# Kernel tuning notes

Measured on AMD Instinct MI355X. Metric: run time of the kernel, lower is better.

Reference implementation:

```python
import jax, jax.numpy as jnp
import numpy as np

NUM_POINTS = 1_000_000
WINDOW = 8                      # 2^3 corner stencil for linear shape functions in 3D
GRID = (128, 128, 128)
NUM_CELLS = GRID[0] * GRID[1] * GRID[2]
CELL = 1.0 / 64.0
INV_CELL = 64.0
ORIGIN = jnp.zeros((3,), dtype=jnp.float32)
# forward_window: the 8 corner offsets of the enclosing cell
FWD_WINDOW = jnp.array([[i, j, k] for i in (0, 1) for j in (0, 1) for k in (0, 1)],
                       dtype=jnp.int32)  # [8,3]


def setup_inputs() -> dict:
    key = jax.random.key(0)
    k1, k2, k3 = jax.random.split(key, 3)
    domain = GRID[0] * CELL
    # keep particles one cell away from the boundary so all stencil hashes are in range
    pos = jax.random.uniform(k1, (NUM_POINTS, 3), dtype=jnp.float32) * (domain - 2 * CELL) + CELL
    vel = jax.random.normal(k2, (NUM_POINTS, 3), dtype=jnp.float32)
    mass = jax.random.uniform(k3, (NUM_POINTS,), dtype=jnp.float32) * 1e-3 + 1e-4
    return {"position_stack": pos, "velocity_stack": vel, "mass_stack": mass}


def reference(position_stack, velocity_stack, mass_stack):
    # ---- get_interactions: gather particle pos, hash into grid, shape functions ----
    rel = (position_stack - ORIGIN) * INV_CELL               # [N,3] position in cell units
    base = jnp.floor(rel)                                    # [N,3]
    grid_pos = base[:, None, :] + FWD_WINDOW[None, :, :].astype(rel.dtype)  # [N,8,3]
    dist = rel[:, None, :] - grid_pos                        # [N,8,3], each dim in (-1,1)

    gp = grid_pos.astype(jnp.int32)
    # get_hash, dim==3: pos[2] + pos[0]*grid[2] + pos[1]*grid[2]*grid[0]
    intr_hash = gp[..., 2] + gp[..., 0] * GRID[2] + gp[..., 1] * (GRID[2] * GRID[0])  # [N,8]

    # linear shape function: N = prod_d (1 - |x_d|); grad scaled by inv_cell_size
    w = 1.0 - jnp.abs(dist)                                  # [N,8,3]
    shapef = w[..., 0] * w[..., 1] * w[..., 2]               # [N,8]
    valid = (intr_hash >= 0) & (intr_hash < NUM_CELLS)
    shapef = jnp.where(valid, shapef, 0.0)

    g0 = -jnp.sign(dist[..., 0]) * w[..., 1] * w[..., 2]
    g1 = -jnp.sign(dist[..., 1]) * w[..., 0] * w[..., 2]
    g2 = -jnp.sign(dist[..., 2]) * w[..., 0] * w[..., 1]
    shapef_grad = jnp.stack([g0, g1, g2], axis=-1) * INV_CELL  # [N,8,3]
    shapef_grad = jnp.where(valid[..., None], shapef_grad, 0.0)

    # intr_dist_padded = -dist * cell_size (kept implicitly via dist; used in APIC-style p2g)
    # ---- p2g scatter (vmap_intr_scatter semantics): mass & momentum to grid nodes ----
    h_flat = jnp.clip(intr_hash, 0, NUM_CELLS - 1).reshape(-1)  # [N*8]
    sm = shapef * mass_stack[:, None]                           # [N,8]
    node_mass = jax.ops.segment_sum(sm.reshape(-1), h_flat, num_segments=NUM_CELLS)   # [C]
    mom = sm[..., None] * velocity_stack[:, None, :]            # [N,8,3]
    node_mom = jax.ops.segment_sum(mom.reshape(-1, 3), h_flat, num_segments=NUM_CELLS)  # [C,3]

    return jnp.concatenate([node_mass[:, None], node_mom], axis=1)  # [C,4]
```

## Files before the change

kernel.cpp:

```cpp
#include <hip/hip_runtime.h>
#include <hip/hip_fp16.h>


#define GRID_DIM   128
#define NUM_CELLS  (GRID_DIM * GRID_DIM * GRID_DIM)
#define INV_CELL   64.0f
#define OVF_MAX    65536
#define SCAN_BLKS  2048

#define TDIM4      32
#define NTILES4    (TDIM4 * TDIM4 * TDIM4)
#define NXCD       8
#define XCAP       16
#define MAXCAP     3
#define NSEG       216
#define NREC       2369
#define EPAD(sc)   ((sc) * 3 + ((sc) >> 2))

typedef float floatx4 __attribute__((ext_vector_type(4)));

__device__ __forceinline__ int cell_id(int ix, int iy, int iz) {
    return iz + ix * GRID_DIM + iy * (GRID_DIM * GRID_DIM);
}

__device__ __forceinline__ unsigned int q16(float f) {
    int q = (int)(f * 65536.0f + 0.5f);
    return (unsigned int)min(q, 65535);
}
__device__ __forceinline__ unsigned int f2h(float f) {
    return (unsigned int)__half_as_ushort(__float2half(f));
}
__device__ __forceinline__ float h2f(unsigned int b) {
    return __half2float(__ushort_as_half((unsigned short)(b & 0xffffu)));
}

__global__ __launch_bounds__(256) void xcd_place_kernel(
    const float* __restrict__ pos, const float* __restrict__ vel,
    const float* __restrict__ mass, unsigned int* __restrict__ tile_cnt,
    uint4* __restrict__ lists, int* __restrict__ ovf_cnt,
    int* __restrict__ ovf_list, int n)
{
    int xcd = blockIdx.x & (NXCD - 1);
    int i0 = blockIdx.x * 512 + threadIdx.x;
    #pragma unroll
    for (int k = 0; k < 2; ++k) {
        int i = i0 + k * 256;
        if (i < n) {
            float px = __builtin_nontemporal_load(&pos[3 * i + 0]);
            float py = __builtin_nontemporal_load(&pos[3 * i + 1]);
            float pz = __builtin_nontemporal_load(&pos[3 * i + 2]);
            float rx = px * INV_CELL, ry = py * INV_CELL, rz = pz * INV_CELL;
            float bx = floorf(rx), by = floorf(ry), bz = floorf(rz);
            float fx = rx - bx, fy = ry - by, fz = rz - bz;
            int ix = min(max((int)bx, 0), GRID_DIM - 1);
            int iy = min(max((int)by, 0), GRID_DIM - 1);
            int iz = min(max((int)bz, 0), GRID_DIM - 1);
            int tile = (iz >> 2) | ((ix >> 2) << 5) | ((iy >> 2) << 10);
            int sub = (xcd << 15) | tile;
            unsigned int s = atomicAdd(&tile_cnt[sub], 1u);
            if (s < (unsigned int)XCAP) {
                float m  = __builtin_nontemporal_load(&mass[i]);
                float vx = __builtin_nontemporal_load(&vel[3 * i + 0]);
                float vy = __builtin_nontemporal_load(&vel[3 * i + 1]);
                float vz = __builtin_nontemporal_load(&vel[3 * i + 2]);
                unsigned int lid = (unsigned int)((iz & 3) | ((ix & 3) << 2)
                                                           | ((iy & 3) << 4));
                uint4 r;
                r.x = q16(fx) | (q16(fy) << 16);
                r.y = q16(fz) | (f2h(m) << 16);
                r.z = f2h(vx) | (f2h(vy) << 16);
                r.w = f2h(vz) | (lid << 16);
                lists[(size_t)sub * XCAP + (int)s] = r;
            } else {
                int o = atomicAdd(ovf_cnt, 1);
                if (o < OVF_MAX) ovf_list[o] = i;
            }
        }
    }
}

__global__ __launch_bounds__(512) void xcd_gather_kernel(
    const uint4* __restrict__ lists, const unsigned int* __restrict__ tile_cnt,
    float4* __restrict__ out)
{
    __shared__ float4 recA[NREC];
    __shared__ unsigned int recB[NREC];
    __shared__ unsigned int cnt_s[729];
    __shared__ unsigned short seg_off[218];
    __shared__ int wtot[8];
    __shared__ int ovf_n;
    __shared__ short ovf_sc[64];
    __shared__ uint4 ovf_rec[64];

    int tid = threadIdx.x;
    int swz = (blockIdx.x & 7) * 512 + (blockIdx.x >> 3);
    int bz = swz & 15;
    int bx = (swz >> 4) & 15;
    int by = swz >> 8;
    int g0x = bx * 8, g0y = by * 8, g0z = bz * 8;
    int Tz0 = bz * 2 - 1, Tx0 = bx * 2 - 1, Ty0 = by * 2 - 1;

    for (int s2 = tid; s2 < 729; s2 += 512) cnt_s[s2] = 0;
    if (tid == 0) ovf_n = 0;

    unsigned int c = 0;
    if (tid < NSEG) {
        int xcd = tid & 7, q = tid >> 3;
        int ltz = q % 3, q2 = q / 3, ltx = q2 % 3, lty = q2 / 3;
        int tz_ = Tz0 + ltz, tx_ = Tx0 + ltx, ty_ = Ty0 + lty;
        if ((tz_ >= 0) & (tx_ >= 0) & (ty_ >= 0)) {
            int tile = tz_ | (tx_ << 5) | (ty_ << 10);
            c = min(tile_cnt[(xcd << 15) | tile], (unsigned int)XCAP);
        }
    }
    unsigned int v = c;
    #pragma unroll
    for (int d = 1; d < 64; d <<= 1) {
        unsigned int t = __shfl_up(v, d, 64);
        if ((tid & 63) >= d) v += t;
    }
    if ((tid & 63) == 63) wtot[tid >> 6] = (int)v;
    __syncthreads();
    if (tid == 0) {
        int run = 0;
        #pragma unroll
        for (int w2 = 0; w2 < 8; ++w2) { int t = wtot[w2]; wtot[w2] = run; run += t; }
    }
    __syncthreads();
    if (tid <= NSEG)
        seg_off[tid] = (unsigned short)((unsigned int)wtot[tid >> 6] + v - c);
    __syncthreads();
    int R = (int)seg_off[NSEG];

    for (int r = tid; r < R; r += 512) {
        int s = 0;
        #pragma unroll
        for (int step = 128; step >= 1; step >>= 1)
            if (s + step <= NSEG && (int)seg_off[s + step] <= r) s += step;
        int xcd = s & 7, q = s >> 3;
        int ltz = q % 3, q2 = q / 3, ltx = q2 % 3, lty = q2 / 3;
        int tz_ = Tz0 + ltz, tx_ = Tx0 + ltx, ty_ = Ty0 + lty;
        int tile = tz_ | (tx_ << 5) | (ty_ << 10);
        int j = r - (int)seg_off[s];
        uint4 rec = lists[(size_t)((xcd << 15) | tile) * XCAP + j];
        unsigned int lid = rec.w >> 16;
        int cz = tz_ * 4 + (int)(lid & 3u);
        int cx = tx_ * 4 + (int)((lid >> 2) & 3u);
        int cy = ty_ * 4 + (int)(lid >> 4);
        int uz = cz - (g0z - 1), ux = cx - (g0x - 1), uy = cy - (g0y - 1);
        if (((unsigned)uz < 9u) & ((unsigned)ux < 9u) & ((unsigned)uy < 9u)) {
            int sc = uy * 81 + ux * 9 + uz;
            unsigned int j2 = atomicAdd(&cnt_s[sc], 1u);
            if (j2 < MAXCAP) {
                int e = EPAD(sc) + (int)j2;
                float fx = (float)(rec.x & 0xffffu) * (1.0f / 65536.0f);
                float fy = (float)(rec.x >> 16)     * (1.0f / 65536.0f);
                float fz = (float)(rec.y & 0xffffu) * (1.0f / 65536.0f);
                recA[e] = make_float4(fx, fy, fz, __uint_as_float(rec.z));
                recB[e] = (rec.y >> 16) | (rec.w << 16);
            } else {
                int o = atomicAdd(&ovf_n, 1);
                if (o < 64) { ovf_sc[o] = (short)sc; ovf_rec[o] = rec; }
            }
        }
    }
    __syncthreads();

    int tz = tid & 7, tx = (tid >> 3) & 7, ty = tid >> 6;
    float a0 = 0.0f, a1 = 0.0f, a2 = 0.0f, a3 = 0.0f;

    #pragma unroll
    for (int dy = 0; dy < 2; ++dy) {
        #pragma unroll
        for (int dx = 0; dx < 2; ++dx) {
            int scb = (ty + dy) * 81 + (tx + dx) * 9 + tz;
            #pragma unroll
            for (int dz = 0; dz < 2; ++dz) {
                int sc = scb + dz;
                int cnt = min((int)cnt_s[sc], MAXCAP);
                int eb = EPAD(sc);
                for (int j = 0; j < cnt; ++j) {
                    float4 A = recA[eb + j];
                    unsigned int B = recB[eb + j];
                    unsigned int w3 = __float_as_uint(A.w);
                    float wx = dx ? (1.0f - A.x) : A.x;
                    float wy = dy ? (1.0f - A.y) : A.y;
                    float wz = dz ? (1.0f - A.z) : A.z;
                    float sm = wx * wy * wz * h2f(B);
                    a0 += sm;
                    a1 += sm * h2f(w3);
                    a2 += sm * h2f(w3 >> 16);
                    a3 += sm * h2f(B >> 16);
                }
            }
        }
    }

    int no = min(ovf_n, 64);
    for (int e2 = 0; e2 < no; ++e2) {
        int sc = (int)ovf_sc[e2];
        int uzv = sc % 9, t2 = sc / 9, uxv = t2 % 9, uyv = t2 / 9;
        int ddz = uzv - tz, ddx = uxv - tx, ddy = uyv - ty;
        if (((unsigned)ddz < 2u) & ((unsigned)ddx < 2u) & ((unsigned)ddy < 2u)) {
            uint4 rec = ovf_rec[e2];
            float fx = (float)(rec.x & 0xffffu) * (1.0f / 65536.0f);
            float fy = (float)(rec.x >> 16)     * (1.0f / 65536.0f);
            float fz = (float)(rec.y & 0xffffu) * (1.0f / 65536.0f);
            float wx = ddx ? (1.0f - fx) : fx;
            float wy = ddy ? (1.0f - fy) : fy;
            float wz = ddz ? (1.0f - fz) : fz;
            float sm = wx * wy * wz * h2f(rec.y >> 16);
            a0 += sm;
            a1 += sm * h2f(rec.z);
            a2 += sm * h2f(rec.z >> 16);
            a3 += sm * h2f(rec.w);
        }
    }

    int id = (g0z + tz) + (g0x + tx) * GRID_DIM
           + (g0y + ty) * (GRID_DIM * GRID_DIM);
    floatx4 vv = { a0, a1, a2, a3 };
    __builtin_nontemporal_store(vv, (floatx4*)&out[id]);
}

__global__ __launch_bounds__(256) void fixup_kernel(
    const float* __restrict__ pos, const float* __restrict__ vel,
    const float* __restrict__ mass, const int* __restrict__ ovf_cnt,
    const int* __restrict__ ovf_list, float* __restrict__ out)
{
    int total = min(*ovf_cnt, OVF_MAX);
    for (int k = blockIdx.x * 256 + threadIdx.x; k < total; k += gridDim.x * 256) {
        int i = ovf_list[k];
        float px = pos[3 * i + 0] * INV_CELL;
        float py = pos[3 * i + 1] * INV_CELL;
        float pz = pos[3 * i + 2] * INV_CELL;
        float bx = floorf(px), by = floorf(py), bz = floorf(pz);
        float fx = px - bx, fy = py - by, fz = pz - bz;
        int ix = (int)bx, iy = (int)by, iz = (int)bz;
        float m = mass[i];
        float vx = vel[3 * i + 0], vy = vel[3 * i + 1], vz = vel[3 * i + 2];
        float wx[2] = { 1.0f - fx, fx }, wy[2] = { 1.0f - fy, fy }, wz[2] = { 1.0f - fz, fz };
        #pragma unroll
        for (int a = 0; a < 2; ++a)
            #pragma unroll
            for (int b = 0; b < 2; ++b)
                #pragma unroll
                for (int c = 0; c < 2; ++c) {
                    int h = cell_id(ix + a, iy + b, iz + c);
                    bool valid = (h >= 0) && (h < NUM_CELLS);
                    int hc = min(max(h, 0), NUM_CELLS - 1);
                    float s = valid ? (wx[a] * wy[b] * wz[c]) : 0.0f;
                    float sm = s * m;
                    float* cell = out + 4 * (size_t)hc;
                    atomicAdd(cell + 0, sm);
                    atomicAdd(cell + 1, sm * vx);
                    atomicAdd(cell + 2, sm * vy);
                    atomicAdd(cell + 3, sm * vz);
                }
    }
}

__global__ __launch_bounds__(256) void s_hist_kernel(
    const float* __restrict__ pos, int* __restrict__ counts, int n)
{
    int i = blockIdx.x * 256 + threadIdx.x;
    if (i >= n) return;
    int ix = min(max((int)floorf(pos[3 * i + 0] * INV_CELL), 0), GRID_DIM - 1);
    int iy = min(max((int)floorf(pos[3 * i + 1] * INV_CELL), 0), GRID_DIM - 1);
    int iz = min(max((int)floorf(pos[3 * i + 2] * INV_CELL), 0), GRID_DIM - 1);
    atomicAdd(&counts[cell_id(ix, iy, iz)], 1);
}

__global__ __launch_bounds__(256) void s_scan_partials_kernel(
    const int* __restrict__ counts, int* __restrict__ partials)
{
    __shared__ int red[256];
    int t = threadIdx.x;
    int4 v = ((const int4*)counts)[blockIdx.x * 256 + t];
    red[t] = v.x + v.y + v.z + v.w;
    __syncthreads();
    for (int off = 128; off > 0; off >>= 1) {
        if (t < off) red[t] += red[t + off];
        __syncthreads();
    }
    if (t == 0) partials[blockIdx.x] = red[0];
}

__global__ __launch_bounds__(1024) void s_scan_tops_kernel(int* __restrict__ partials)
{
    __shared__ int s[1024];
    int t = threadIdx.x;
    int p0 = partials[2 * t], p1 = partials[2 * t + 1];
    int sum = p0 + p1;
    s[t] = sum;
    __syncthreads();
    for (int off = 1; off < 1024; off <<= 1) {
        int x = (t >= off) ? s[t - off] : 0;
        __syncthreads();
        s[t] += x;
        __syncthreads();
    }
    int excl = s[t] - sum;
    partials[2 * t] = excl;
    partials[2 * t + 1] = excl + p0;
}

__global__ __launch_bounds__(256) void s_scan_final_kernel(
    const int* __restrict__ counts, const int* __restrict__ partials,
    int* __restrict__ offsets, int* __restrict__ cursors)
{
    __shared__ int s[256];
    int t = threadIdx.x;
    int g = blockIdx.x * 256 + t;
    int4 v = ((const int4*)counts)[g];
    int sum = v.x + v.y + v.z + v.w;
    s[t] = sum;
    __syncthreads();
    for (int off = 1; off < 256; off <<= 1) {
        int x = (t >= off) ? s[t - off] : 0;
        __syncthreads();
        s[t] += x;
        __syncthreads();
    }
    int run = partials[blockIdx.x] + s[t] - sum;
    int4 o = make_int4(run, run + v.x, run + v.x + v.y, run + v.x + v.y + v.z);
    ((int4*)offsets)[g] = o;
    ((int4*)cursors)[g] = o;
}

__global__ __launch_bounds__(256) void s_binplace_kernel(
    const float* __restrict__ pos, const float* __restrict__ vel,
    const float* __restrict__ mass, int* __restrict__ cursors,
    float4* __restrict__ records, int n)
{
    int i = blockIdx.x * 256 + threadIdx.x;
    if (i >= n) return;
    float rx = pos[3 * i + 0] * INV_CELL;
    float ry = pos[3 * i + 1] * INV_CELL;
    float rz = pos[3 * i + 2] * INV_CELL;
    int ix = min(max((int)floorf(rx), 0), GRID_DIM - 1);
    int iy = min(max((int)floorf(ry), 0), GRID_DIM - 1);
    int iz = min(max((int)floorf(rz), 0), GRID_DIM - 1);
    int slot = atomicAdd(&cursors[cell_id(ix, iy, iz)], 1);
    records[2 * slot + 0] = make_float4(rx, ry, rz, mass[i]);
    records[2 * slot + 1] = make_float4(vel[3 * i + 0], vel[3 * i + 1],
                                        vel[3 * i + 2], 0.0f);
}

__global__ __launch_bounds__(256) void s_node_gather_kernel(
    const float4* __restrict__ records, const int* __restrict__ offsets,
    const int* __restrict__ cursors, float4* __restrict__ out)
{
    int id = blockIdx.x * 256 + threadIdx.x;
    int gz = id & (GRID_DIM - 1);
    int gx = (id >> 7) & (GRID_DIM - 1);
    int gy = id >> 14;
    float fgx = (float)gx, fgy = (float)gy, fgz = (float)gz;
    float a0 = 0.0f, a1 = 0.0f, a2 = 0.0f, a3 = 0.0f;
    int z0 = max(gz - 1, 0), y0 = max(gy - 1, 0), x0 = max(gx - 1, 0);
    for (int cy = y0; cy <= gy; ++cy) {
        for (int cx = x0; cx <= gx; ++cx) {
            int cb = cx * GRID_DIM + cy * (GRID_DIM * GRID_DIM);
            int beg = offsets[cb + z0];
            int end = cursors[cb + gz];
            for (int p = beg; p < end; ++p) {
                float4 r0 = records[2 * p + 0];
                float4 r1 = records[2 * p + 1];
                float w = (1.0f - fabsf(r0.x - fgx)) *
                          (1.0f - fabsf(r0.y - fgy)) *
                          (1.0f - fabsf(r0.z - fgz));
                float sm = w * r0.w;
                a0 += sm; a1 += sm * r1.x; a2 += sm * r1.y; a3 += sm * r1.z;
            }
        }
    }
    out[id] = make_float4(a0, a1, a2, a3);
}

__global__ __launch_bounds__(256) void p2g_scatter_kernel(
    const float* __restrict__ pos, const float* __restrict__ vel,
    const float* __restrict__ mass, float* __restrict__ out, int n)
{
    int i = blockIdx.x * blockDim.x + threadIdx.x;
    if (i >= n) return;
    float px = pos[3 * i + 0] * INV_CELL;
    float py = pos[3 * i + 1] * INV_CELL;
    float pz = pos[3 * i + 2] * INV_CELL;
    float bx = floorf(px), by = floorf(py), bz = floorf(pz);
    float fx = px - bx, fy = py - by, fz = pz - bz;
    int ix = (int)bx, iy = (int)by, iz = (int)bz;
    float m = mass[i];
    float vx = vel[3 * i + 0], vy = vel[3 * i + 1], vz = vel[3 * i + 2];
    float wx[2] = { 1.0f - fx, fx }, wy[2] = { 1.0f - fy, fy }, wz[2] = { 1.0f - fz, fz };
    #pragma unroll
    for (int a = 0; a < 2; ++a)
        #pragma unroll
        for (int b = 0; b < 2; ++b)
            #pragma unroll
            for (int c = 0; c < 2; ++c) {
                int h = cell_id(ix + a, iy + b, iz + c);
                bool valid = (h >= 0) && (h < NUM_CELLS);
                int hc = min(max(h, 0), NUM_CELLS - 1);
                float s = valid ? (wx[a] * wy[b] * wz[c]) : 0.0f;
                float sm = s * m;
                float* cell = out + 4 * (size_t)hc;
                atomicAdd(cell + 0, sm);
                atomicAdd(cell + 1, sm * vx);
                atomicAdd(cell + 2, sm * vy);
                atomicAdd(cell + 3, sm * vz);
            }
}

extern "C" void kernel_launch(void* const* d_in, const int* in_sizes, int n_in,
                              void* d_out, int out_size, void* d_ws, size_t ws_size,
                              hipStream_t stream) {
    const float* pos  = (const float*)d_in[0];
    const float* vel  = (const float*)d_in[1];
    const float* mass = (const float*)d_in[2];
    float* out = (float*)d_out;
    int n = in_sizes[2];
    int blocks = (n + 255) / 256;

    size_t x_off_lists = (size_t)NXCD * NTILES4 * 4;
    size_t x_off_ovf   = x_off_lists + (size_t)NXCD * NTILES4 * XCAP * 16;
    size_t need_xcd    = x_off_ovf + 256 + (size_t)OVF_MAX * 4;

    size_t s_off_offsets  = (size_t)NUM_CELLS * 4;
    size_t s_off_records  = s_off_offsets + (size_t)NUM_CELLS * 4;
    size_t s_off_partials = s_off_records + (size_t)n * 32;
    size_t need_sorted    = s_off_partials + (size_t)SCAN_BLKS * 4;

    if (ws_size >= need_xcd) {
        char* ws = (char*)d_ws;
        unsigned int* tile_cnt = (unsigned int*)ws;
        uint4* lists  = (uint4*)(ws + x_off_lists);
        int* ovf_cnt  = (int*)(ws + x_off_ovf);
        int* ovf_list = ovf_cnt + 64;

        (void)hipMemsetAsync(tile_cnt, 0, x_off_lists, stream);
        (void)hipMemsetAsync(ovf_cnt, 0, 4, stream);
        xcd_place_kernel<<<(n + 511) / 512, 256, 0, stream>>>(
            pos, vel, mass, tile_cnt, lists, ovf_cnt, ovf_list, n);
        xcd_gather_kernel<<<NTILES4 / 8, 512, 0, stream>>>(
            lists, tile_cnt, (float4*)out);
        fixup_kernel<<<32, 256, 0, stream>>>(pos, vel, mass, ovf_cnt,
                                             ovf_list, out);
    } else if (ws_size >= need_sorted) {
        char* ws = (char*)d_ws;
        int* counts   = (int*)ws;
        int* offsets  = (int*)(ws + s_off_offsets);
        float4* records = (float4*)(ws + s_off_records);
        int* partials = (int*)(ws + s_off_partials);

        (void)hipMemsetAsync(counts, 0, (size_t)NUM_CELLS * 4, stream);
        s_hist_kernel<<<blocks, 256, 0, stream>>>(pos, counts, n);
        s_scan_partials_kernel<<<SCAN_BLKS, 256, 0, stream>>>(counts, partials);
        s_scan_tops_kernel<<<1, 1024, 0, stream>>>(partials);
        s_scan_final_kernel<<<SCAN_BLKS, 256, 0, stream>>>(counts, partials,
                                                           offsets, counts);
        s_binplace_kernel<<<blocks, 256, 0, stream>>>(pos, vel, mass, counts,
                                                      records, n);
        s_node_gather_kernel<<<NUM_CELLS / 256, 256, 0, stream>>>(
            records, offsets, counts, (float4*)out);
    } else {
        (void)hipMemsetAsync(out, 0, (size_t)out_size * sizeof(float), stream);
        p2g_scatter_kernel<<<blocks, 256, 0, stream>>>(pos, vel, mass, out, n);
    }
}
```

Before: 175.7 us.

## Replace fixed-capacity tile lists with counting-sort dense lists via histogram and scan

Replaces the per-(XCD,tile) fixed 16-slot lists, and the overflow list with its atomic fixup kernel, with a counting sort. A histogram pass over positions is followed by a three-kernel prefix scan and a placement pass into densely packed records. The gather kernel reads each segment's base offset and count from the offsets and cursors arrays. This removes the overflow path and shrinks the list footprint from a padded 16-slot-per-tile array to one record per particle. In exchange it adds a second pass over the positions and four more kernel launches.

After: 206.7 us. +17.6%, slower.

```diff
diff --git a/kernel.cpp b/kernel.cpp
--- a/kernel.cpp
+++ b/kernel.cpp
@@ -5,13 +5,12 @@
 #define GRID_DIM   128
 #define NUM_CELLS  (GRID_DIM * GRID_DIM * GRID_DIM)
 #define INV_CELL   64.0f
-#define OVF_MAX    65536
 #define SCAN_BLKS  2048
 
 #define TDIM4      32
 #define NTILES4    (TDIM4 * TDIM4 * TDIM4)
 #define NXCD       8
-#define XCAP       16
+#define NSUB       (NXCD * NTILES4)
 #define MAXCAP     3
 #define NSEG       216
 #define NREC       2369
@@ -34,59 +33,119 @@
     return __half2float(__ushort_as_half((unsigned short)(b & 0xffffu)));
 }
 
-__global__ __launch_bounds__(256) void xcd_place_kernel(
+__global__ __launch_bounds__(256) void x_hist_kernel(
+    const float* __restrict__ pos, unsigned int* __restrict__ tile_cnt, int n)
+{
+    int xcd = blockIdx.x & (NXCD - 1);
+    int i = blockIdx.x * 256 + threadIdx.x;
+    if (i >= n) return;
+    float px = __builtin_nontemporal_load(&pos[3 * i + 0]);
+    float py = __builtin_nontemporal_load(&pos[3 * i + 1]);
+    float pz = __builtin_nontemporal_load(&pos[3 * i + 2]);
+    int ix = min(max((int)floorf(px * INV_CELL), 0), GRID_DIM - 1);
+    int iy = min(max((int)floorf(py * INV_CELL), 0), GRID_DIM - 1);
+    int iz = min(max((int)floorf(pz * INV_CELL), 0), GRID_DIM - 1);
+    int tile = (iz >> 2) | ((ix >> 2) << 5) | ((iy >> 2) << 10);
+    atomicAdd(&tile_cnt[(xcd << 15) | tile], 1u);
+}
+
+__global__ __launch_bounds__(256) void x_scan_partials(
+    const unsigned int* __restrict__ cnt, unsigned int* __restrict__ partials)
+{
+    __shared__ unsigned int red[256];
+    int t = threadIdx.x;
+    uint4 v = ((const uint4*)cnt)[blockIdx.x * 256 + t];
+    red[t] = v.x + v.y + v.z + v.w;
+    __syncthreads();
+    for (int off = 128; off > 0; off >>= 1) {
+        if (t < off) red[t] += red[t + off];
+        __syncthreads();
+    }
+    if (t == 0) partials[blockIdx.x] = red[0];
+}
+
+__global__ __launch_bounds__(256) void x_scan_tops(unsigned int* __restrict__ partials)
+{
+    __shared__ unsigned int s[256];
+    int t = threadIdx.x;
+    unsigned int p = partials[t];
+    s[t] = p;
+    __syncthreads();
+    for (int off = 1; off < 256; off <<= 1) {
+        unsigned int x = (t >= off) ? s[t - off] : 0;
+        __syncthreads();
+        s[t] += x;
+        __syncthreads();
+    }
+    partials[t] = s[t] - p;
+}
+
+__global__ __launch_bounds__(256) void x_scan_final(
+    const unsigned int* __restrict__ cnt, const unsigned int* __restrict__ partials,
+    unsigned int* __restrict__ offsets, unsigned int* __restrict__ cursors)
+{
+    __shared__ unsigned int s[256];
+    int t = threadIdx.x;
+    int g = blockIdx.x * 256 + t;
+    uint4 v = ((const uint4*)cnt)[g];
+    unsigned int sum = v.x + v.y + v.z + v.w;
+    s[t] = sum;
+    __syncthreads();
+    for (int off = 1; off < 256; off <<= 1) {
+        unsigned int x = (t >= off) ? s[t - off] : 0;
+        __syncthreads();
+        s[t] += x;
+        __syncthreads();
+    }
+    unsigned int run = partials[blockIdx.x] + s[t] - sum;
+    uint4 o = make_uint4(run, run + v.x, run + v.x + v.y, run + v.x + v.y + v.z);
+    ((uint4*)offsets)[g] = o;
+    ((uint4*)cursors)[g] = o;
+}
+
+__global__ __launch_bounds__(256) void xcd_binplace_kernel(
     const float* __restrict__ pos, const float* __restrict__ vel,
-    const float* __restrict__ mass, unsigned int* __restrict__ tile_cnt,
-    uint4* __restrict__ lists, int* __restrict__ ovf_cnt,
-    int* __restrict__ ovf_list, int n)
+    const float* __restrict__ mass, unsigned int* __restrict__ cursors,
+    uint4* __restrict__ lists, int n)
 {
     int xcd = blockIdx.x & (NXCD - 1);
-    int i0 = blockIdx.x * 512 + threadIdx.x;
-    #pragma unroll
-    for (int k = 0; k < 2; ++k) {
-        int i = i0 + k * 256;
-        if (i < n) {
-            float px = __builtin_nontemporal_load(&pos[3 * i + 0]);
-            float py = __builtin_nontemporal_load(&pos[3 * i + 1]);
-            float pz = __builtin_nontemporal_load(&pos[3 * i + 2]);
-            float rx = px * INV_CELL, ry = py * INV_CELL, rz = pz * INV_CELL;
-            float bx = floorf(rx), by = floorf(ry), bz = floorf(rz);
-            float fx = rx - bx, fy = ry - by, fz = rz - bz;
-            int ix = min(max((int)bx, 0), GRID_DIM - 1);
-            int iy = min(max((int)by, 0), GRID_DIM - 1);
-            int iz = min(max((int)bz, 0), GRID_DIM - 1);
-            int tile = (iz >> 2) | ((ix >> 2) << 5) | ((iy >> 2) << 10);
-            int sub = (xcd << 15) | tile;
-            unsigned int s = atomicAdd(&tile_cnt[sub], 1u);
-            if (s < (unsigned int)XCAP) {
-                float m  = __builtin_nontemporal_load(&mass[i]);
-                float vx = __builtin_nontemporal_load(&vel[3 * i + 0]);
-                float vy = __builtin_nontemporal_load(&vel[3 * i + 1]);
-                float vz = __builtin_nontemporal_load(&vel[3 * i + 2]);
-                unsigned int lid = (unsigned int)((iz & 3) | ((ix & 3) << 2)
-                                                           | ((iy & 3) << 4));
-                uint4 r;
-                r.x = q16(fx) | (q16(fy) << 16);
-                r.y = q16(fz) | (f2h(m) << 16);
-                r.z = f2h(vx) | (f2h(vy) << 16);
-                r.w = f2h(vz) | (lid << 16);
-                lists[(size_t)sub * XCAP + (int)s] = r;
-            } else {
-                int o = atomicAdd(ovf_cnt, 1);
-                if (o < OVF_MAX) ovf_list[o] = i;
-            }
-        }
-    }
+    int i = blockIdx.x * 256 + threadIdx.x;
+    if (i >= n) return;
+    float px = __builtin_nontemporal_load(&pos[3 * i + 0]);
+    float py = __builtin_nontemporal_load(&pos[3 * i + 1]);
+    float pz = __builtin_nontemporal_load(&pos[3 * i + 2]);
+    float rx = px * INV_CELL, ry = py * INV_CELL, rz = pz * INV_CELL;
+    float bx = floorf(rx), by = floorf(ry), bz = floorf(rz);
+    float fx = rx - bx, fy = ry - by, fz = rz - bz;
+    int ix = min(max((int)bx, 0), GRID_DIM - 1);
+    int iy = min(max((int)by, 0), GRID_DIM - 1);
+    int iz = min(max((int)bz, 0), GRID_DIM - 1);
+    int tile = (iz >> 2) | ((ix >> 2) << 5) | ((iy >> 2) << 10);
+    int sub = (xcd << 15) | tile;
+    unsigned int s = atomicAdd(&cursors[sub], 1u);
+    float m  = __builtin_nontemporal_load(&mass[i]);
+    float vx = __builtin_nontemporal_load(&vel[3 * i + 0]);
+    float vy = __builtin_nontemporal_load(&vel[3 * i + 1]);
+    float vz = __builtin_nontemporal_load(&vel[3 * i + 2]);
+    unsigned int lid = (unsigned int)((iz & 3) | ((ix & 3) << 2)
+                                               | ((iy & 3) << 4));
+    uint4 r;
+    r.x = q16(fx) | (q16(fy) << 16);
+    r.y = q16(fz) | (f2h(m) << 16);
+    r.z = f2h(vx) | (f2h(vy) << 16);
+    r.w = f2h(vz) | (lid << 16);
+    lists[s] = r;
 }
 
 __global__ __launch_bounds__(512) void xcd_gather_kernel(
-    const uint4* __restrict__ lists, const unsigned int* __restrict__ tile_cnt,
-    float4* __restrict__ out)
+    const uint4* __restrict__ lists, const unsigned int* __restrict__ offsets,
+    const unsigned int* __restrict__ cursors, float4* __restrict__ out)
 {
     __shared__ float4 recA[NREC];
     __shared__ unsigned int recB[NREC];
     __shared__ unsigned int cnt_s[729];
-    __shared__ unsigned short seg_off[218];
+    __shared__ unsigned int seg_base[NSEG];
+    __shared__ unsigned int seg_off[218];
     __shared__ int wtot[8];
     __shared__ int ovf_n;
     __shared__ short ovf_sc[64];
@@ -103,14 +162,15 @@
     for (int s2 = tid; s2 < 729; s2 += 512) cnt_s[s2] = 0;
     if (tid == 0) ovf_n = 0;
 
-    unsigned int c = 0;
+    unsigned int c = 0, base = 0;
     if (tid < NSEG) {
         int xcd = tid & 7, q = tid >> 3;
         int ltz = q % 3, q2 = q / 3, ltx = q2 % 3, lty = q2 / 3;
         int tz_ = Tz0 + ltz, tx_ = Tx0 + ltx, ty_ = Ty0 + lty;
         if ((tz_ >= 0) & (tx_ >= 0) & (ty_ >= 0)) {
-            int tile = tz_ | (tx_ << 5) | (ty_ << 10);
-            c = min(tile_cnt[(xcd << 15) | tile], (unsigned int)XCAP);
+            int sub = (xcd << 15) | (tz_ | (tx_ << 5) | (ty_ << 10));
+            base = offsets[sub];
+            c = cursors[sub] - base;
         }
     }
     unsigned int v = c;
@@ -128,7 +188,8 @@
     }
     __syncthreads();
     if (tid <= NSEG)
-        seg_off[tid] = (unsigned short)((unsigned int)wtot[tid >> 6] + v - c);
+        seg_off[tid] = (unsigned int)wtot[tid >> 6] + v - c;
+    if (tid < NSEG) seg_base[tid] = base;
     __syncthreads();
     int R = (int)seg_off[NSEG];
 
@@ -137,12 +198,11 @@
         #pragma unroll
         for (int step = 128; step >= 1; step >>= 1)
             if (s + step <= NSEG && (int)seg_off[s + step] <= r) s += step;
-        int xcd = s & 7, q = s >> 3;
+        int q = s >> 3;
         int ltz = q % 3, q2 = q / 3, ltx = q2 % 3, lty = q2 / 3;
         int tz_ = Tz0 + ltz, tx_ = Tx0 + ltx, ty_ = Ty0 + lty;
-        int tile = tz_ | (tx_ << 5) | (ty_ << 10);
         int j = r - (int)seg_off[s];
-        uint4 rec = lists[(size_t)((xcd << 15) | tile) * XCAP + j];
+        uint4 rec = lists[seg_base[s] + j];
         unsigned int lid = rec.w >> 16;
         int cz = tz_ * 4 + (int)(lid & 3u);
         int cx = tx_ * 4 + (int)((lid >> 2) & 3u);
@@ -221,43 +281,6 @@
            + (g0y + ty) * (GRID_DIM * GRID_DIM);
     floatx4 vv = { a0, a1, a2, a3 };
     __builtin_nontemporal_store(vv, (floatx4*)&out[id]);
-}
-
-__global__ __launch_bounds__(256) void fixup_kernel(
-    const float* __restrict__ pos, const float* __restrict__ vel,
-    const float* __restrict__ mass, const int* __restrict__ ovf_cnt,
-    const int* __restrict__ ovf_list, float* __restrict__ out)
-{
-    int total = min(*ovf_cnt, OVF_MAX);
-    for (int k = blockIdx.x * 256 + threadIdx.x; k < total; k += gridDim.x * 256) {
-        int i = ovf_list[k];
-        float px = pos[3 * i + 0] * INV_CELL;
-        float py = pos[3 * i + 1] * INV_CELL;
-        float pz = pos[3 * i + 2] * INV_CELL;
-        float bx = floorf(px), by = floorf(py), bz = floorf(pz);
-        float fx = px - bx, fy = py - by, fz = pz - bz;
-        int ix = (int)bx, iy = (int)by, iz = (int)bz;
-        float m = mass[i];
-        float vx = vel[3 * i + 0], vy = vel[3 * i + 1], vz = vel[3 * i + 2];
-        float wx[2] = { 1.0f - fx, fx }, wy[2] = { 1.0f - fy, fy }, wz[2] = { 1.0f - fz, fz };
-        #pragma unroll
-        for (int a = 0; a < 2; ++a)
-            #pragma unroll
-            for (int b = 0; b < 2; ++b)
-                #pragma unroll
-                for (int c = 0; c < 2; ++c) {
-                    int h = cell_id(ix + a, iy + b, iz + c);
-                    bool valid = (h >= 0) && (h < NUM_CELLS);
-                    int hc = min(max(h, 0), NUM_CELLS - 1);
-                    float s = valid ? (wx[a] * wy[b] * wz[c]) : 0.0f;
-                    float sm = s * m;
-                    float* cell = out + 4 * (size_t)hc;
-                    atomicAdd(cell + 0, sm);
-                    atomicAdd(cell + 1, sm * vx);
-                    atomicAdd(cell + 2, sm * vy);
-                    atomicAdd(cell + 3, sm * vz);
-                }
-    }
 }
 
 __global__ __launch_bounds__(256) void s_hist_kernel(
@@ -421,30 +444,35 @@
     int n = in_sizes[2];
     int blocks = (n + 255) / 256;
 
-    size_t x_off_lists = (size_t)NXCD * NTILES4 * 4;
-    size_t x_off_ovf   = x_off_lists + (size_t)NXCD * NTILES4 * XCAP * 16;
-    size_t need_xcd    = x_off_ovf + 256 + (size_t)OVF_MAX * 4;
+    size_t x_off_offsets  = (size_t)NSUB * 4;
+    size_t x_off_cursors  = x_off_offsets + (size_t)NSUB * 4;
+    size_t x_off_partials = x_off_cursors + (size_t)NSUB * 4;
+    size_t x_off_lists    = x_off_partials + 4096;
+    size_t need_dense     = x_off_lists + (size_t)n * 16;
 
     size_t s_off_offsets  = (size_t)NUM_CELLS * 4;
     size_t s_off_records  = s_off_offsets + (size_t)NUM_CELLS * 4;
     size_t s_off_partials = s_off_records + (size_t)n * 32;
     size_t need_sorted    = s_off_partials + (size_t)SCAN_BLKS * 4;
 
-    if (ws_size >= need_xcd) {
+    if (ws_size >= need_dense) {
         char* ws = (char*)d_ws;
         unsigned int* tile_cnt = (unsigned int*)ws;
-        uint4* lists  = (uint4*)(ws + x_off_lists);
-        int* ovf_cnt  = (int*)(ws + x_off_ovf);
-        int* ovf_list = ovf_cnt + 64;
-
-        (void)hipMemsetAsync(tile_cnt, 0, x_off_lists, stream);
-        (void)hipMemsetAsync(ovf_cnt, 0, 4, stream);
-        xcd_place_kernel<<<(n + 511) / 512, 256, 0, stream>>>(
-            pos, vel, mass, tile_cnt, lists, ovf_cnt, ovf_list, n);
+        unsigned int* offsets  = (unsigned int*)(ws + x_off_offsets);
+        unsigned int* cursors  = (unsigned int*)(ws + x_off_cursors);
+        unsigned int* partials = (unsigned int*)(ws + x_off_partials);
+        uint4* lists           = (uint4*)(ws + x_off_lists);
+
+        (void)hipMemsetAsync(tile_cnt, 0, (size_t)NSUB * 4, stream);
+        x_hist_kernel<<<blocks, 256, 0, stream>>>(pos, tile_cnt, n);
+        x_scan_partials<<<NSUB / 1024, 256, 0, stream>>>(tile_cnt, partials);
+        x_scan_tops<<<1, 256, 0, stream>>>(partials);
+        x_scan_final<<<NSUB / 1024, 256, 0, stream>>>(tile_cnt, partials,
+                                                      offsets, cursors);
+        xcd_binplace_kernel<<<blocks, 256, 0, stream>>>(
+            pos, vel, mass, cursors, lists, n);
         xcd_gather_kernel<<<NTILES4 / 8, 512, 0, stream>>>(
-            lists, tile_cnt, (float4*)out);
-        fixup_kernel<<<32, 256, 0, stream>>>(pos, vel, mass, ovf_cnt,
-                                             ovf_list, out);
+            lists, offsets, cursors, (float4*)out);
     } else if (ws_size >= need_sorted) {
         char* ws = (char*)d_ws;
         int* counts   = (int*)ws;
```

## Replace per-XCD tile lists with two-pass region binning and in-region tile sort

Applied to the files above, without the earlier changes.

Drops the per-XCD 4^3 tile lists, which used scattered global atomics and fixed-capacity slots. Each block now bins 4096 particles into 512 coarse 16^3-cell regions in LDS and writes them to global region buffers in contiguous chunks, with one global atomic per region per block. A second kernel sorts each region's records into 64 tiles, so the gather reads 27 contiguous segments instead of 216 small per-XCD lists. Overflow records are stored packed, so fixup no longer re-reads the original inputs. The cost is an extra kernel pass that reads and writes all records, plus heavy LDS use.

After: 163.5 us. -6.9%, faster.

```diff
diff --git a/kernel.cpp b/kernel.cpp
--- a/kernel.cpp
+++ b/kernel.cpp
@@ -8,12 +8,11 @@
 #define OVF_MAX    65536
 #define SCAN_BLKS  2048
 
-#define TDIM4      32
-#define NTILES4    (TDIM4 * TDIM4 * TDIM4)
-#define NXCD       8
-#define XCAP       16
+#define NREG       512
+#define RCAP       2560
+#define PPB        4096
 #define MAXCAP     3
-#define NSEG       216
+#define NSEG       27
 #define NREC       2369
 #define EPAD(sc)   ((sc) * 3 + ((sc) >> 2))
 
@@ -34,18 +33,34 @@
     return __half2float(__ushort_as_half((unsigned short)(b & 0xffffu)));
 }
 
-__global__ __launch_bounds__(256) void xcd_place_kernel(
+__global__ __launch_bounds__(1024) void region_bin_kernel(
     const float* __restrict__ pos, const float* __restrict__ vel,
-    const float* __restrict__ mass, unsigned int* __restrict__ tile_cnt,
-    uint4* __restrict__ lists, int* __restrict__ ovf_cnt,
-    int* __restrict__ ovf_list, int n)
-{
-    int xcd = blockIdx.x & (NXCD - 1);
-    int i0 = blockIdx.x * 512 + threadIdx.x;
+    const float* __restrict__ mass, unsigned int* __restrict__ region_cursor,
+    uint4* __restrict__ regbuf, int* __restrict__ ovf_cnt,
+    uint4* __restrict__ ovf_rec, unsigned int* __restrict__ ovf_reg, int n)
+{
+    __shared__ uint4 rec_lds[PPB];
+    __shared__ unsigned short regof[PPB];
+    __shared__ unsigned int cnt[NREG];
+    __shared__ unsigned int lofs[NREG];
+    __shared__ unsigned int gbase[NREG];
+    __shared__ unsigned int wtot[8];
+
+    int tid = threadIdx.x;
+    int base_i = blockIdx.x * PPB;
+    int blockn = min(PPB, n - base_i);
+
+    if (tid < NREG) cnt[tid] = 0;
+    __syncthreads();
+
+    uint4 r_[4]; int reg_[4], rank_[4], val_[4];
     #pragma unroll
-    for (int k = 0; k < 2; ++k) {
-        int i = i0 + k * 256;
-        if (i < n) {
+    for (int k = 0; k < 4; ++k) {
+        int e = k * 1024 + tid;
+        int i = base_i + e;
+        val_[k] = (e < blockn);
+        reg_[k] = 0; rank_[k] = 0;
+        if (val_[k]) {
             float px = __builtin_nontemporal_load(&pos[3 * i + 0]);
             float py = __builtin_nontemporal_load(&pos[3 * i + 1]);
             float pz = __builtin_nontemporal_load(&pos[3 * i + 2]);
@@ -55,39 +70,137 @@
             int ix = min(max((int)bx, 0), GRID_DIM - 1);
             int iy = min(max((int)by, 0), GRID_DIM - 1);
             int iz = min(max((int)bz, 0), GRID_DIM - 1);
-            int tile = (iz >> 2) | ((ix >> 2) << 5) | ((iy >> 2) << 10);
-            int sub = (xcd << 15) | tile;
-            unsigned int s = atomicAdd(&tile_cnt[sub], 1u);
-            if (s < (unsigned int)XCAP) {
-                float m  = __builtin_nontemporal_load(&mass[i]);
-                float vx = __builtin_nontemporal_load(&vel[3 * i + 0]);
-                float vy = __builtin_nontemporal_load(&vel[3 * i + 1]);
-                float vz = __builtin_nontemporal_load(&vel[3 * i + 2]);
-                unsigned int lid = (unsigned int)((iz & 3) | ((ix & 3) << 2)
-                                                           | ((iy & 3) << 4));
-                uint4 r;
-                r.x = q16(fx) | (q16(fy) << 16);
-                r.y = q16(fz) | (f2h(m) << 16);
-                r.z = f2h(vx) | (f2h(vy) << 16);
-                r.w = f2h(vz) | (lid << 16);
-                lists[(size_t)sub * XCAP + (int)s] = r;
-            } else {
-                int o = atomicAdd(ovf_cnt, 1);
-                if (o < OVF_MAX) ovf_list[o] = i;
-            }
-        }
-    }
-}
-
-__global__ __launch_bounds__(512) void xcd_gather_kernel(
-    const uint4* __restrict__ lists, const unsigned int* __restrict__ tile_cnt,
+            int reg = (iz >> 4) | ((ix >> 4) << 3) | ((iy >> 4) << 6);
+            unsigned int cid = (unsigned int)((iz & 15) | ((ix & 15) << 4)
+                                                        | ((iy & 15) << 8));
+            float m  = __builtin_nontemporal_load(&mass[i]);
+            float vx = __builtin_nontemporal_load(&vel[3 * i + 0]);
+            float vy = __builtin_nontemporal_load(&vel[3 * i + 1]);
+            float vz = __builtin_nontemporal_load(&vel[3 * i + 2]);
+            uint4 r;
+            r.x = q16(fx) | (q16(fy) << 16);
+            r.y = q16(fz) | (f2h(m) << 16);
+            r.z = f2h(vx) | (f2h(vy) << 16);
+            r.w = f2h(vz) | (cid << 16);
+            r_[k] = r;
+            reg_[k] = reg;
+            rank_[k] = (int)atomicAdd(&cnt[reg], 1u);
+        }
+    }
+    __syncthreads();
+
+    unsigned int c = 0, v = 0;
+    if (tid < NREG) {
+        c = cnt[tid];
+        v = c;
+        #pragma unroll
+        for (int d = 1; d < 64; d <<= 1) {
+            unsigned int t = __shfl_up(v, d, 64);
+            if ((tid & 63) >= d) v += t;
+        }
+        if ((tid & 63) == 63) wtot[tid >> 6] = v;
+    }
+    __syncthreads();
+    if (tid == 0) {
+        unsigned int run = 0;
+        #pragma unroll
+        for (int w = 0; w < 8; ++w) { unsigned int t = wtot[w]; wtot[w] = run; run += t; }
+    }
+    __syncthreads();
+    if (tid < NREG) {
+        lofs[tid] = wtot[tid >> 6] + v - c;
+        if (c) gbase[tid] = atomicAdd(&region_cursor[tid], c);
+    }
+    __syncthreads();
+
+    #pragma unroll
+    for (int k = 0; k < 4; ++k) {
+        if (val_[k]) {
+            int d = (int)lofs[reg_[k]] + rank_[k];
+            rec_lds[d] = r_[k];
+            regof[d] = (unsigned short)reg_[k];
+        }
+    }
+    __syncthreads();
+
+    for (int e = tid; e < blockn; e += 1024) {
+        uint4 rr = rec_lds[e];
+        int rg = (int)regof[e];
+        unsigned int slot = gbase[rg] + (unsigned int)(e - (int)lofs[rg]);
+        if (slot < (unsigned int)RCAP) {
+            regbuf[(size_t)rg * RCAP + slot] = rr;
+        } else {
+            int o = atomicAdd(ovf_cnt, 1);
+            if (o < OVF_MAX) { ovf_rec[o] = rr; ovf_reg[o] = (unsigned int)rg; }
+        }
+    }
+}
+
+__global__ __launch_bounds__(1024) void tile_sort_kernel(
+    uint4* __restrict__ regbuf, const unsigned int* __restrict__ region_cursor,
+    unsigned int* __restrict__ tile_off)
+{
+    __shared__ uint4 out_lds[RCAP];
+    __shared__ unsigned int cnt64[64];
+    __shared__ unsigned int tofs[65];
+
+    int r = blockIdx.x;
+    int tid = threadIdx.x;
+    int cntR = (int)min(region_cursor[r], (unsigned int)RCAP);
+
+    if (tid < 64) cnt64[tid] = 0;
+    __syncthreads();
+
+    uint4 rr_[3]; int t_[3], rk_[3], vl_[3];
+    #pragma unroll
+    for (int k = 0; k < 3; ++k) {
+        int e = k * 1024 + tid;
+        vl_[k] = (e < cntR);
+        t_[k] = 0; rk_[k] = 0;
+        if (vl_[k]) {
+            uint4 rr = regbuf[(size_t)r * RCAP + e];
+            unsigned int cid = rr.w >> 16;
+            int t = (int)(((cid & 15u) >> 2) | ((((cid >> 4) & 15u) >> 2) << 2)
+                                             | ((((cid >> 8) & 15u) >> 2) << 4));
+            rr_[k] = rr;
+            t_[k] = t;
+            rk_[k] = (int)atomicAdd(&cnt64[t], 1u);
+        }
+    }
+    __syncthreads();
+
+    if (tid < 64) {
+        unsigned int c = cnt64[tid], v = c;
+        #pragma unroll
+        for (int d = 1; d < 64; d <<= 1) {
+            unsigned int t = __shfl_up(v, d, 64);
+            if (tid >= d) v += t;
+        }
+        tofs[tid] = v - c;
+        if (tid == 63) tofs[64] = v;
+    }
+    __syncthreads();
+
+    #pragma unroll
+    for (int k = 0; k < 3; ++k)
+        if (vl_[k]) out_lds[(int)tofs[t_[k]] + rk_[k]] = rr_[k];
+    __syncthreads();
+
+    for (int e = tid; e < cntR; e += 1024)
+        regbuf[(size_t)r * RCAP + e] = out_lds[e];
+    if (tid < 65) tile_off[r * 65 + tid] = tofs[tid];
+}
+
+__global__ __launch_bounds__(512) void tile_gather2_kernel(
+    const uint4* __restrict__ regbuf, const unsigned int* __restrict__ tile_off,
     float4* __restrict__ out)
 {
     __shared__ float4 recA[NREC];
     __shared__ unsigned int recB[NREC];
     __shared__ unsigned int cnt_s[729];
-    __shared__ unsigned short seg_off[218];
-    __shared__ int wtot[8];
+    __shared__ unsigned int seg_gb[NSEG];
+    __shared__ unsigned short seg_reg[NSEG];
+    __shared__ unsigned int seg_off[NSEG + 1];
     __shared__ int ovf_n;
     __shared__ short ovf_sc[64];
     __shared__ uint4 ovf_rec[64];
@@ -103,50 +216,47 @@
     for (int s2 = tid; s2 < 729; s2 += 512) cnt_s[s2] = 0;
     if (tid == 0) ovf_n = 0;
 
-    unsigned int c = 0;
-    if (tid < NSEG) {
-        int xcd = tid & 7, q = tid >> 3;
-        int ltz = q % 3, q2 = q / 3, ltx = q2 % 3, lty = q2 / 3;
-        int tz_ = Tz0 + ltz, tx_ = Tx0 + ltx, ty_ = Ty0 + lty;
-        if ((tz_ >= 0) & (tx_ >= 0) & (ty_ >= 0)) {
-            int tile = tz_ | (tx_ << 5) | (ty_ << 10);
-            c = min(tile_cnt[(xcd << 15) | tile], (unsigned int)XCAP);
-        }
-    }
-    unsigned int v = c;
-    #pragma unroll
-    for (int d = 1; d < 64; d <<= 1) {
-        unsigned int t = __shfl_up(v, d, 64);
-        if ((tid & 63) >= d) v += t;
-    }
-    if ((tid & 63) == 63) wtot[tid >> 6] = (int)v;
-    __syncthreads();
-    if (tid == 0) {
-        int run = 0;
-        #pragma unroll
-        for (int w2 = 0; w2 < 8; ++w2) { int t = wtot[w2]; wtot[w2] = run; run += t; }
-    }
-    __syncthreads();
-    if (tid <= NSEG)
-        seg_off[tid] = (unsigned short)((unsigned int)wtot[tid >> 6] + v - c);
+    if (tid < 64) {
+        unsigned int c = 0;
+        if (tid < NSEG) {
+            int ltz = tid % 3, q = tid / 3, ltx = q % 3, lty = q / 3;
+            int Tz = Tz0 + ltz, Tx = Tx0 + ltx, Ty = Ty0 + lty;
+            unsigned int gb = 0; int reg = 0;
+            if ((Tz >= 0) & (Tx >= 0) & (Ty >= 0)) {
+                reg = (Tz >> 2) | ((Tx >> 2) << 3) | ((Ty >> 2) << 6);
+                int tl = (Tz & 3) | ((Tx & 3) << 2) | ((Ty & 3) << 4);
+                unsigned int o0 = tile_off[reg * 65 + tl];
+                unsigned int o1 = tile_off[reg * 65 + tl + 1];
+                c = o1 - o0;
+                gb = (unsigned int)reg * RCAP + o0;
+            }
+            seg_reg[tid] = (unsigned short)reg;
+            seg_gb[tid] = gb;
+        }
+        unsigned int v = c;
+        #pragma unroll
+        for (int d = 1; d < 64; d <<= 1) {
+            unsigned int t = __shfl_up(v, d, 64);
+            if (tid >= d) v += t;
+        }
+        if (tid < NSEG) seg_off[tid] = v - c;
+        if (tid == NSEG - 1) seg_off[NSEG] = v;
+    }
     __syncthreads();
     int R = (int)seg_off[NSEG];
 
     for (int r = tid; r < R; r += 512) {
         int s = 0;
         #pragma unroll
-        for (int step = 128; step >= 1; step >>= 1)
+        for (int step = 16; step >= 1; step >>= 1)
             if (s + step <= NSEG && (int)seg_off[s + step] <= r) s += step;
-        int xcd = s & 7, q = s >> 3;
-        int ltz = q % 3, q2 = q / 3, ltx = q2 % 3, lty = q2 / 3;
-        int tz_ = Tz0 + ltz, tx_ = Tx0 + ltx, ty_ = Ty0 + lty;
-        int tile = tz_ | (tx_ << 5) | (ty_ << 10);
         int j = r - (int)seg_off[s];
-        uint4 rec = lists[(size_t)((xcd << 15) | tile) * XCAP + j];
-        unsigned int lid = rec.w >> 16;
-        int cz = tz_ * 4 + (int)(lid & 3u);
-        int cx = tx_ * 4 + (int)((lid >> 2) & 3u);
-        int cy = ty_ * 4 + (int)(lid >> 4);
+        uint4 rec = regbuf[seg_gb[s] + j];
+        unsigned int cid = rec.w >> 16;
+        int reg = (int)seg_reg[s];
+        int cz = (reg & 7) * 16 + (int)(cid & 15u);
+        int cx = ((reg >> 3) & 7) * 16 + (int)((cid >> 4) & 15u);
+        int cy = ((reg >> 6) & 7) * 16 + (int)((cid >> 8) & 15u);
         int uz = cz - (g0z - 1), ux = cx - (g0x - 1), uy = cy - (g0y - 1);
         if (((unsigned)uz < 9u) & ((unsigned)ux < 9u) & ((unsigned)uy < 9u)) {
             int sc = uy * 81 + ux * 9 + uz;
@@ -223,22 +333,23 @@
     __builtin_nontemporal_store(vv, (floatx4*)&out[id]);
 }
 
-__global__ __launch_bounds__(256) void fixup_kernel(
-    const float* __restrict__ pos, const float* __restrict__ vel,
-    const float* __restrict__ mass, const int* __restrict__ ovf_cnt,
-    const int* __restrict__ ovf_list, float* __restrict__ out)
+__global__ __launch_bounds__(256) void fixup_packed_kernel(
+    const int* __restrict__ ovf_cnt, const uint4* __restrict__ ovf_rec,
+    const unsigned int* __restrict__ ovf_reg, float* __restrict__ out)
 {
     int total = min(*ovf_cnt, OVF_MAX);
     for (int k = blockIdx.x * 256 + threadIdx.x; k < total; k += gridDim.x * 256) {
-        int i = ovf_list[k];
-        float px = pos[3 * i + 0] * INV_CELL;
-        float py = pos[3 * i + 1] * INV_CELL;
-        float pz = pos[3 * i + 2] * INV_CELL;
-        float bx = floorf(px), by = floorf(py), bz = floorf(pz);
-        float fx = px - bx, fy = py - by, fz = pz - bz;
-        int ix = (int)bx, iy = (int)by, iz = (int)bz;
-        float m = mass[i];
-        float vx = vel[3 * i + 0], vy = vel[3 * i + 1], vz = vel[3 * i + 2];
+        uint4 rec = ovf_rec[k];
+        unsigned int reg = ovf_reg[k];
+        unsigned int cid = rec.w >> 16;
+        int iz = (int)(reg & 7u) * 16 + (int)(cid & 15u);
+        int ix = (int)((reg >> 3) & 7u) * 16 + (int)((cid >> 4) & 15u);
+        int iy = (int)((reg >> 6) & 7u) * 16 + (int)((cid >> 8) & 15u);
+        float fx = (float)(rec.x & 0xffffu) * (1.0f / 65536.0f);
+        float fy = (float)(rec.x >> 16)     * (1.0f / 65536.0f);
+        float fz = (float)(rec.y & 0xffffu) * (1.0f / 65536.0f);
+        float m  = h2f(rec.y >> 16);
+        float vx = h2f(rec.z), vy = h2f(rec.z >> 16), vz = h2f(rec.w);
         float wx[2] = { 1.0f - fx, fx }, wy[2] = { 1.0f - fy, fy }, wz[2] = { 1.0f - fz, fz };
         #pragma unroll
         for (int a = 0; a < 2; ++a)
@@ -421,30 +532,37 @@
     int n = in_sizes[2];
     int blocks = (n + 255) / 256;
 
-    size_t x_off_lists = (size_t)NXCD * NTILES4 * 4;
-    size_t x_off_ovf   = x_off_lists + (size_t)NXCD * NTILES4 * XCAP * 16;
-    size_t need_xcd    = x_off_ovf + 256 + (size_t)OVF_MAX * 4;
+    size_t w_off_tileoff = 4096;
+    size_t w_off_ovfcnt  = w_off_tileoff + (size_t)NREG * 65 * 4;
+    size_t w_off_ovfrec  = w_off_ovfcnt + 256;
+    size_t w_off_ovfreg  = w_off_ovfrec + (size_t)OVF_MAX * 16;
+    size_t w_off_regbuf  = w_off_ovfreg + (size_t)OVF_MAX * 4;
+    size_t need_twopass  = w_off_regbuf + (size_t)NREG * RCAP * 16;
 
     size_t s_off_offsets  = (size_t)NUM_CELLS * 4;
     size_t s_off_records  = s_off_offsets + (size_t)NUM_CELLS * 4;
     size_t s_off_partials = s_off_records + (size_t)n * 32;
     size_t need_sorted    = s_off_partials + (size_t)SCAN_BLKS * 4;
 
-    if (ws_size >= need_xcd) {
+    if (ws_size >= need_twopass) {
         char* ws = (char*)d_ws;
-        unsigned int* tile_cnt = (unsigned int*)ws;
-        uint4* lists  = (uint4*)(ws + x_off_lists);
-        int* ovf_cnt  = (int*)(ws + x_off_ovf);
-        int* ovf_list = ovf_cnt + 64;
-
-        (void)hipMemsetAsync(tile_cnt, 0, x_off_lists, stream);
+        unsigned int* region_cursor = (unsigned int*)ws;
+        unsigned int* tile_off = (unsigned int*)(ws + w_off_tileoff);
+        int* ovf_cnt           = (int*)(ws + w_off_ovfcnt);
+        uint4* ovf_rec         = (uint4*)(ws + w_off_ovfrec);
+        unsigned int* ovf_reg  = (unsigned int*)(ws + w_off_ovfreg);
+        uint4* regbuf          = (uint4*)(ws + w_off_regbuf);
+
+        (void)hipMemsetAsync(region_cursor, 0, (size_t)NREG * 4, stream);
         (void)hipMemsetAsync(ovf_cnt, 0, 4, stream);
-        xcd_place_kernel<<<(n + 511) / 512, 256, 0, stream>>>(
-            pos, vel, mass, tile_cnt, lists, ovf_cnt, ovf_list, n);
-        xcd_gather_kernel<<<NTILES4 / 8, 512, 0, stream>>>(
-            lists, tile_cnt, (float4*)out);
-        fixup_kernel<<<32, 256, 0, stream>>>(pos, vel, mass, ovf_cnt,
-                                             ovf_list, out);
+        region_bin_kernel<<<(n + PPB - 1) / PPB, 1024, 0, stream>>>(
+            pos, vel, mass, region_cursor, regbuf, ovf_cnt, ovf_rec, ovf_reg, n);
+        tile_sort_kernel<<<NREG, 1024, 0, stream>>>(regbuf, region_cursor,
+                                                    tile_off);
+        tile_gather2_kernel<<<4096, 512, 0, stream>>>(regbuf, tile_off,
+                                                      (float4*)out);
+        fixup_packed_kernel<<<16, 256, 0, stream>>>(ovf_cnt, ovf_rec,
+                                                    ovf_reg, out);
     } else if (ws_size >= need_sorted) {
         char* ws = (char*)d_ws;
         int* counts   = (int*)ws;
```
